# Kernel tuning notes

Measured on AMD Instinct MI355X. Metric: run time of the kernel, lower is better.

The kernel has to match this reference:

```python
import jax, jax.numpy as jnp
import numpy as np

N_IMG = 8
IMG_H = IMG_W = 1024
STRIDES = (4, 8, 16, 32, 64)
FEAT = tuple(IMG_H // s for s in STRIDES)
RATIOS = (0.5, 1.0, 2.0)
A = len(RATIOS)
PRE_NMS = 1000
POST_NMS = 1000
NMS_THRESH = 0.7
SCORE_THRESH = 0.0
MIN_SIZE = 1e-3
BBOX_CLIP = float(np.log(1000.0 / 16.0))  # torchvision bbox_xform_clip
NPL = tuple(f * f * A for f in FEAT)      # anchors per level


def _make_anchors():
    levels = []
    for stride, f in zip(STRIDES, FEAT):
        size = stride * 8.0
        base = []
        for r in RATIOS:
            w = size * np.sqrt(1.0 / r)
            h = size * np.sqrt(r)
            base.append([-w / 2, -h / 2, w / 2, h / 2])
        base = np.asarray(base, np.float32)              # [A,4]
        coords = np.arange(f, dtype=np.float32) * stride
        sy, sx = np.meshgrid(coords, coords, indexing="ij")
        shifts = np.stack([sx, sy, sx, sy], -1).reshape(-1, 1, 4)  # y-major, matches [H,W,A] flatten
        levels.append((shifts + base[None]).reshape(-1, 4))
    return np.concatenate(levels, 0).astype(np.float32)


def setup_inputs() -> dict:
    key = jax.random.key(0)
    ks = jax.random.split(key, 10)
    inp = {}
    for i, f in enumerate(FEAT):
        inp[f"obj_l{i}"] = jax.random.normal(ks[i], (N_IMG, A, f, f), jnp.float32)
        inp[f"delta_l{i}"] = jax.random.normal(ks[5 + i], (N_IMG, A * 4, f, f), jnp.float32) * 0.2
    inp["anchors"] = jnp.asarray(_make_anchors())
    return inp


def _flatten_level(obj, delta):
    # permute_and_flatten: [N,A,H,W] -> [N,H*W*A] ; [N,A*4,H,W] -> [N,H*W*A,4]
    n, a, h, w = obj.shape
    o = jnp.transpose(obj, (0, 2, 3, 1)).reshape(n, -1)
    d = jnp.transpose(delta.reshape(n, a, 4, h, w), (0, 3, 4, 1, 2)).reshape(n, -1, 4)
    return o, d


def _decode(deltas, anchors):
    # BoxCoder(weights=(1,1,1,1)).decode
    w = anchors[:, 2] - anchors[:, 0]
    h = anchors[:, 3] - anchors[:, 1]
    cx = anchors[:, 0] + 0.5 * w
    cy = anchors[:, 1] + 0.5 * h
    dx, dy = deltas[..., 0], deltas[..., 1]
    dw = jnp.minimum(deltas[..., 2], BBOX_CLIP)
    dh = jnp.minimum(deltas[..., 3], BBOX_CLIP)
    pcx = dx * w + cx
    pcy = dy * h + cy
    pw = jnp.exp(dw) * w
    ph = jnp.exp(dh) * h
    return jnp.stack([pcx - 0.5 * pw, pcy - 0.5 * ph, pcx + 0.5 * pw, pcy + 0.5 * ph], -1)


def _nms_image(boxes, scores, lvl):
    # clip_boxes_to_image
    x1 = jnp.clip(boxes[:, 0], 0.0, IMG_W)
    y1 = jnp.clip(boxes[:, 1], 0.0, IMG_H)
    x2 = jnp.clip(boxes[:, 2], 0.0, IMG_W)
    y2 = jnp.clip(boxes[:, 3], 0.0, IMG_H)
    boxes = jnp.stack([x1, y1, x2, y2], -1)
    # remove_small_boxes + score_thresh, as a mask (fixed shapes)
    valid = (x2 - x1 >= MIN_SIZE) & (y2 - y1 >= MIN_SIZE) & (scores >= SCORE_THRESH)
    s = jnp.where(valid, scores, -1.0)
    order = jnp.argsort(-s)
    boxes, s, valid, lvl = boxes[order], s[order], valid[order], lvl[order]
    # batched_nms: offset boxes per level so cross-level IoU is 0
    ob = boxes + (lvl.astype(boxes.dtype) * (max(IMG_H, IMG_W) + 1.0))[:, None]
    ob = jax.lax.stop_gradient(ob)  # keep decisions are non-differentiable
    area = (ob[:, 2] - ob[:, 0]) * (ob[:, 3] - ob[:, 1])
    lt = jnp.maximum(ob[:, None, :2], ob[None, :, :2])
    rb = jnp.minimum(ob[:, None, 2:], ob[None, :, 2:])
    wh = jnp.maximum(rb - lt, 0.0)
    inter = wh[..., 0] * wh[..., 1]
    iou = inter / (area[:, None] + area[None, :] - inter + 1e-9)  # [K,K]
    k = boxes.shape[0]
    jidx = jnp.arange(k)

    def body(i, keep):
        sup = keep[i] & (iou[i] > NMS_THRESH) & (jidx > i)
        return keep & ~sup

    keep = jax.lax.fori_loop(0, k, body, valid)
    # compact kept boxes (score-sorted) into fixed [POST_NMS] output, zero-padded
    rank = jnp.cumsum(keep) - 1
    tgt = jnp.where(keep & (rank < POST_NMS), rank, POST_NMS)
    out_b = jnp.zeros((POST_NMS + 1, 4), boxes.dtype).at[tgt].set(boxes)[:POST_NMS]
    out_s = jnp.zeros((POST_NMS + 1,), s.dtype).at[tgt].set(jnp.where(keep, s, 0.0))[:POST_NMS]
    return out_b, out_s


def _forward(objs, deltas, anchors):
    flat = [_flatten_level(o, d) for o, d in zip(objs, deltas)]
    obj = jnp.concatenate([f[0] for f in flat], 1)       # [N, K_total]
    dl = jnp.concatenate([f[1] for f in flat], 1)        # [N, K_total, 4]
    proposals = _decode(dl, anchors)                     # [N, K_total, 4]
    lvl_full = jnp.concatenate([jnp.full((n,), i, jnp.int32) for i, n in enumerate(NPL)])
    # per-level top-k on objectness logits
    idxs, off = [], 0
    for n in NPL:
        kk = min(PRE_NMS, n)
        _, ti = jax.lax.top_k(obj[:, off:off + n], kk)
        idxs.append(ti + off)
        off += n
    top_idx = jnp.concatenate(idxs, 1)                   # [N, K_sel]
    scores = jax.nn.sigmoid(jnp.take_along_axis(obj, top_idx, 1))
    prop = jnp.take_along_axis(proposals, top_idx[..., None], 1)
    lvl = lvl_full[top_idx]
    boxes_out, _ = jax.lax.map(lambda t: _nms_image(*t), (prop, scores, lvl))
    return boxes_out                                     # [N, POST_NMS, 4]


def reference(obj_l0, obj_l1, obj_l2, obj_l3, obj_l4, delta_l0, delta_l1, delta_l2, delta_l3, delta_l4, anchors):
    return _forward([obj_l0, obj_l1, obj_l2, obj_l3, obj_l4],
                    [delta_l0, delta_l1, delta_l2, delta_l3, delta_l4], anchors)
```

## Files before the change

### kernel.cpp

```cpp
#include <hip/hip_runtime.h>
#include <cstdint>

#define K_SEL 4768
#define CAND_CAP 16384
#define NBIN 4096
#define BUFCAP 512

struct P5 { const float* p[5]; };

__device__ __forceinline__ unsigned fsortkey(float f) {
  unsigned b = __float_as_uint(f);
  return (b & 0x80000000u) ? ~b : (b | 0x80000000u);
}

__global__ __launch_bounds__(256) void k_hist(P5 obj, unsigned* phist) {
  int p = blockIdx.y; int img = p / 5, lvl = p % 5;
  int f = 256 >> lvl; int n = 3 * f * f;
  __shared__ unsigned lh[NBIN];
  for (int b = threadIdx.x; b < NBIN; b += 256) lh[b] = 0;
  __syncthreads();
  const float4* src4 = (const float4*)(obj.p[lvl] + (size_t)img * n);
  int n4 = n >> 2;
  int chunk = (n4 + gridDim.x - 1) / gridDim.x;
  int e0 = blockIdx.x * chunk, e1 = min(n4, e0 + chunk);
  for (int e = e0 + threadIdx.x; e < e1; e += 256) {
    float4 v = src4[e];
    atomicAdd(&lh[fsortkey(v.x) >> 20], 1u);
    atomicAdd(&lh[fsortkey(v.y) >> 20], 1u);
    atomicAdd(&lh[fsortkey(v.z) >> 20], 1u);
    atomicAdd(&lh[fsortkey(v.w) >> 20], 1u);
  }
  __syncthreads();
  unsigned* dst = phist + ((size_t)(p * 8 + blockIdx.x)) * NBIN;
  for (int b = threadIdx.x; b < NBIN; b += 256) dst[b] = lh[b];
}

__global__ __launch_bounds__(256) void k_thresh(const unsigned* phist, int* Bthr, unsigned* cnt) {
  int p = blockIdx.x; int lvl = p % 5;
  unsigned kk = (lvl == 4) ? 768u : 1000u;
  __shared__ unsigned hsum[NBIN];
  __shared__ unsigned csum[256];
  int c = threadIdx.x;
  unsigned tot[16];
#pragma unroll
  for (int k = 0; k < 16; ++k) tot[k] = 0;
  for (int g = 0; g < 8; ++g) {
    const unsigned* hp = phist + ((size_t)(p * 8 + g)) * NBIN + c * 16;
#pragma unroll
    for (int k = 0; k < 16; ++k) tot[k] += hp[k];
  }
  unsigned s = 0;
#pragma unroll
  for (int k = 0; k < 16; ++k) { hsum[c * 16 + k] = tot[k]; s += tot[k]; }
  csum[c] = s;
  __syncthreads();
  if (c == 0) {
    unsigned acc = 0; int B = 0;
    for (int cc = 255; cc >= 0; --cc) {
      if (acc + csum[cc] >= kk) {
        for (int b = 15; b >= 0; --b) {
          acc += hsum[cc * 16 + b];
          if (acc >= kk) { B = cc * 16 + b; break; }
        }
        break;
      }
      acc += csum[cc];
    }
    Bthr[p] = B;
    cnt[p] = 0;
  }
}

__global__ __launch_bounds__(256) void k_gather(P5 obj, const int* Bthr, unsigned* cnt,
                                                unsigned long long* ck) {
  int p = blockIdx.y; int img = p / 5, lvl = p % 5;
  int f = 256 >> lvl; int hw = f * f; int n = 3 * hw;
  int B = Bthr[p];
  int shift = 2 * (8 - lvl);
  const float4* src4 = (const float4*)(obj.p[lvl] + (size_t)img * n);
  int n4 = n >> 2;
  unsigned long long* dst = ck + (size_t)p * CAND_CAP;
  int tid = threadIdx.x;
  int lane = tid & 63, wv = tid >> 6;
  __shared__ unsigned long long buf[4][BUFCAP];
  __shared__ unsigned wTot[4];
  __shared__ unsigned blkBase;
  unsigned wc = 0;
  for (int e = blockIdx.x * 256 + tid; e < n4; e += gridDim.x * 256) {
    float4 v = src4[e];
    float vv[4] = {v.x, v.y, v.z, v.w};
#pragma unroll
    for (int j = 0; j < 4; ++j) {
      unsigned sv = fsortkey(vv[j]);
      bool pass = (int)(sv >> 20) >= B;
      unsigned long long m = __ballot(pass);
      if (m) {
        if (pass) {
          unsigned pos = wc + (unsigned)__popcll(m & ((1ULL << lane) - 1ULL));
          int ee = e * 4 + j;
          int a = ee >> shift;
          int r = ee & (hw - 1);
          unsigned kidx = (unsigned)(r * 3 + a);
          unsigned long long key = ((unsigned long long)sv << 32) | (0xFFFFFFFFu - kidx);
          if (pos < BUFCAP) buf[wv][pos] = key;
          else {
            unsigned gp = atomicAdd(&cnt[p], 1u);
            if (gp < CAND_CAP) dst[gp] = key;
          }
        }
        wc += (unsigned)__popcll(m);
      }
    }
  }
  if (lane == 0) wTot[wv] = min(wc, (unsigned)BUFCAP);
  __syncthreads();
  if (tid == 0) {
    unsigned tot = wTot[0] + wTot[1] + wTot[2] + wTot[3];
    blkBase = tot ? atomicAdd(&cnt[p], tot) : 0u;
  }
  __syncthreads();
  unsigned myOff = blkBase;
  for (int x = 0; x < wv; ++x) myOff += wTot[x];
  unsigned wn = wTot[wv];
  for (unsigned j = lane; j < wn; j += 64) {
    unsigned gp = myOff + j;
    if (gp < CAND_CAP) dst[gp] = buf[wv][j];
  }
}

__global__ __launch_bounds__(256) void k_select(const unsigned* cnt, const unsigned long long* ck,
                                                unsigned* selSV, unsigned* selIdx) {
  int p = blockIdx.y; int img = p / 5, lvl = p % 5;
  int Cc = min((int)cnt[p], CAND_CAP);
  if (blockIdx.x * 256 >= Cc) return;
  int kk = (lvl == 4) ? 768 : 1000;
  int soff = lvl * 1000;
  const unsigned long long* keys = ck + (size_t)p * CAND_CAP;
  __shared__ unsigned long long sk[4096];
  int stage = min(Cc, 4096);
  for (int j = threadIdx.x; j < stage; j += 256) sk[j] = keys[j];
  __syncthreads();
  int c = blockIdx.x * 256 + threadIdx.x;
  if (c >= Cc) return;
  unsigned long long kc = keys[c];
  int rank = 0;
#pragma unroll 8
  for (int j = 0; j < stage; ++j) rank += (sk[j] > kc) ? 1 : 0;
  for (int j = stage; j < Cc; ++j) rank += (keys[j] > kc) ? 1 : 0;
  if (rank < kk) {
    int slot = img * K_SEL + soff + rank;
    selSV[slot]  = (unsigned)(kc >> 32);
    selIdx[slot] = 0xFFFFFFFFu - (unsigned)kc;
  }
}

__global__ __launch_bounds__(256) void k_decode(P5 del, const float* anchors,
                                                const unsigned* selSV, const unsigned* selIdx,
                                                float* boxP, unsigned long long* keyP) {
  int i = blockIdx.x * 256 + threadIdx.x;
  if (i >= K_SEL) return;
  int img = blockIdx.y;
  int lvl = (i < 4000) ? (i / 1000) : 4;
  int f = 256 >> lvl, hw = f * f;
  const int aoffA[5] = {0, 196608, 245760, 258048, 261120};
  int slot = img * K_SEL + i;
  unsigned k = selIdx[slot];
  unsigned sv = selSV[slot];
  int a = (int)(k % 3u); int r = (int)(k / 3u);
  int y = r >> (8 - lvl); int x = r & (f - 1);
  const float* dp = del.p[lvl] + (size_t)(img * 12 + a * 4) * hw + (size_t)y * f + x;
  float d0 = dp[0], d1 = dp[hw], d2 = dp[2 * hw], d3 = dp[3 * hw];
  const float* ar = anchors + (size_t)(aoffA[lvl] + (int)k) * 4;
  float a0 = ar[0], a1 = ar[1], a2 = ar[2], a3 = ar[3];
  float w = __fsub_rn(a2, a0), h = __fsub_rn(a3, a1);
  float cx = __fadd_rn(a0, __fmul_rn(0.5f, w));
  float cy = __fadd_rn(a1, __fmul_rn(0.5f, h));
  const float CLIP = 4.135166556742356f;
  float dw = fminf(d2, CLIP), dh = fminf(d3, CLIP);
  float pcx = __fadd_rn(__fmul_rn(d0, w), cx);
  float pcy = __fadd_rn(__fmul_rn(d1, h), cy);
  float pw = __fmul_rn(expf(dw), w);
  float ph = __fmul_rn(expf(dh), h);
  float x1 = __fsub_rn(pcx, __fmul_rn(0.5f, pw));
  float y1 = __fsub_rn(pcy, __fmul_rn(0.5f, ph));
  float x2 = __fadd_rn(pcx, __fmul_rn(0.5f, pw));
  float y2 = __fadd_rn(pcy, __fmul_rn(0.5f, ph));
  float x1c = fminf(fmaxf(x1, 0.0f), 1024.0f);
  float y1c = fminf(fmaxf(y1, 0.0f), 1024.0f);
  float x2c = fminf(fmaxf(x2, 0.0f), 1024.0f);
  float y2c = fminf(fmaxf(y2, 0.0f), 1024.0f);
  bool valid = (__fsub_rn(x2c, x1c) >= 1e-3f) && (__fsub_rn(y2c, y1c) >= 1e-3f);
  float* bp = boxP + (size_t)slot * 4;
  bp[0] = x1c; bp[1] = y1c; bp[2] = x2c; bp[3] = y2c;
  unsigned low = 0xFFFFFFFFu - (unsigned)i;
  keyP[slot] = valid ? (((unsigned long long)sv << 32) | low) : (unsigned long long)low;
}

__device__ __forceinline__ bool iou_gt(float rx1, float ry1, float rx2, float ry2, float rar,
                                       float cx1, float cy1, float cx2, float cy2, float car) {
  float ltx = fmaxf(rx1, cx1), lty = fmaxf(ry1, cy1);
  float rbx = fminf(rx2, cx2), rby = fminf(ry2, cy2);
  float wx = fmaxf(__fsub_rn(rbx, ltx), 0.0f);
  float wy = fmaxf(__fsub_rn(rby, lty), 0.0f);
  float inter = __fmul_rn(wx, wy);
  float denom = __fadd_rn(__fsub_rn(__fadd_rn(rar, car), inter), 1e-9f);
  return __fdiv_rn(inter, denom) > 0.7f;
}

__global__ __launch_bounds__(64) void k_lvlmask(const float* boxP, unsigned long long* gmask,
                                                unsigned long long* diagT) {
  int img = blockIdx.y;
  int q = blockIdx.x;
  int lvl, q2;
  if (q < 544) { lvl = q / 136; q2 = q - lvl * 136; }
  else         { lvl = 4;       q2 = q - 544; }
  int kk = (lvl == 4) ? 768 : 1000;
  int nch = (kk + 63) >> 6;
  int rb = 0;
  while (q2 >= nch - rb) { q2 -= nch - rb; ++rb; }
  int cb = rb + q2;
  int t = threadIdx.x;
  float off = __fmul_rn((float)lvl, 1025.0f);
  const float4* b4 = (const float4*)boxP + (size_t)img * K_SEL + lvl * 1000;
  __shared__ float cx1[64], cy1[64], cx2[64], cy2[64], car[64];
  int j = cb * 64 + t;
  if (j < kk) {
    float4 bb = b4[j];
    float ox1 = __fadd_rn(bb.x, off), oy1 = __fadd_rn(bb.y, off);
    float ox2 = __fadd_rn(bb.z, off), oy2 = __fadd_rn(bb.w, off);
    cx1[t] = ox1; cy1[t] = oy1; cx2[t] = ox2; cy2[t] = oy2;
    car[t] = __fmul_rn(__fsub_rn(ox2, ox1), __fsub_rn(oy2, oy1));
  }
  __syncthreads();
  int i = rb * 64 + t;
  if (i >= kk) return;
  float4 bb = b4[i];
  float rx1 = __fadd_rn(bb.x, off), ry1 = __fadd_rn(bb.y, off);
  float rx2 = __fadd_rn(bb.z, off), ry2 = __fadd_rn(bb.w, off);
  float rar = __fmul_rn(__fsub_rn(rx2, rx1), __fsub_rn(ry2, ry1));
  unsigned long long bits = 0;
  int jmax = min(64, kk - cb * 64);
  if (rb == cb) {
    unsigned long long bitsT = 0;
    for (int jj = 0; jj < jmax; ++jj) {
      if (jj == t) continue;
      if (iou_gt(rx1, ry1, rx2, ry2, rar, cx1[jj], cy1[jj], cx2[jj], cy2[jj], car[jj])) {
        if (jj > t) bits  |= (1ULL << jj);
        else        bitsT |= (1ULL << jj);
      }
    }
    diagT[((size_t)(img * 5 + lvl) * 16 + rb) * 64 + t] = bitsT;
  } else {
    for (int jj = 0; jj < jmax; ++jj) {
      if (iou_gt(rx1, ry1, rx2, ry2, rar, cx1[jj], cy1[jj], cx2[jj], cy2[jj], car[jj]))
        bits |= (1ULL << jj);
    }
  }
  gmask[((size_t)(img * 5 + lvl) * 1000 + i) * 16 + cb] = bits;
}

__global__ __launch_bounds__(64, 1) void k_lvlnms(const unsigned long long* keyP,
                                                  const unsigned long long* gmask,
                                                  const unsigned long long* diagT,
                                                  unsigned long long* keepw) {
  int p = blockIdx.x; int img = p / 5, lvl = p % 5;
  int kk = (lvl == 4) ? 768 : 1000;
  int nch = (kk + 63) >> 6;
  int t = threadIdx.x;
  int g = t >> 4, w = t & 15;
  const unsigned long long* gm = gmask + (size_t)p * 16000;
  const unsigned long long* kp = keyP + (size_t)img * K_SEL + lvl * 1000;
  const unsigned long long* dT = diagT + (size_t)p * (16 * 64);
  unsigned long long rp = 0ULL;
  int i0 = min(t, kk - 1);
  unsigned long long vpre = kp[i0];
  unsigned long long tpre = dT[t];
  for (int c = 0; c < nch; ++c) {
    int cbase = c * 64;
    const unsigned long long* sb = gm + (size_t)(cbase + g) * 16 + w;
    unsigned long long spec[16];
#pragma unroll
    for (int k = 0; k < 16; ++k) spec[k] = sb[k * 64];
    int i = cbase + t;
    bool inb = i < kk;
    bool cand0 = inb && (vpre >> 32) != 0ULL;
    unsigned long long colT = tpre;
    int cn = (c + 1 < nch) ? c + 1 : c;
    int inx = min(cn * 64 + t, kk - 1);
    vpre = kp[inx];
    tpre = dT[cn * 64 + t];
    unsigned long long cur = __shfl(rp, c) | __shfl(rp, 16 + c) |
                             __shfl(rp, 32 + c) | __shfl(rp, 48 + c);
    bool alive = cand0 && !((cur >> t) & 1ULL);
    unsigned long long keepm = 0ULL;
    unsigned long long actm = __ballot(alive);
    while (actm) {
      bool cank = alive && ((colT & actm) == 0ULL);
      unsigned long long newk = __ballot(cank);
      keepm |= newk;
      alive = alive && !cank && ((colT & newk) == 0ULL);
      actm = __ballot(alive);
    }
    if (t == 0) keepw[(size_t)p * 16 + c] = keepm;
    if (c + 1 == nch) break;
#pragma unroll
    for (int k = 0; k < 16; ++k)
      rp |= ((keepm >> (4 * k + g)) & 1ULL) ? spec[k] : 0ULL;
  }
}

__global__ __launch_bounds__(256) void k_merge(const unsigned long long* keyP, const float* boxP,
                                               const unsigned long long* keepw, float* out) {
  int p = blockIdx.x; int img = p / 5, lvl = p % 5;
  int tid = threadIdx.x;
  __shared__ unsigned long long lkey[5000];
  __shared__ int lpos[5000];
  __shared__ int wp[5][17];
  __shared__ unsigned long long kwS[80];
  for (int x = tid; x < 80; x += 256) {
    int l = x >> 4, w = x & 15;
    kwS[x] = (l == 4 && w >= 12) ? 0ULL : keepw[(size_t)img * 80 + x];
  }
  __syncthreads();
  if (tid < 5) {
    int acc = 0;
    for (int w = 0; w < 16; ++w) { wp[tid][w] = acc; acc += (int)__popcll(kwS[tid * 16 + w]); }
    wp[tid][16] = acc;
  }
  __syncthreads();
  const unsigned long long* kp = keyP + (size_t)img * K_SEL;
  for (int i = tid; i < K_SEL; i += 256) {
    int l = (i < 4000) ? i / 1000 : 4;
    int li = i - l * 1000;
    unsigned long long wmask = kwS[l * 16 + (li >> 6)];
    if ((wmask >> (li & 63)) & 1ULL) {
      int j = wp[l][li >> 6] + (int)__popcll(wmask & ((1ULL << (li & 63)) - 1ULL));
      lkey[l * 1000 + j] = kp[i];
      lpos[l * 1000 + j] = i;
    }
  }
  __syncthreads();
  const float4* b4 = (const float4*)boxP + (size_t)img * K_SEL;
  float4* out4 = (float4*)out + (size_t)img * 1000;
  int kn = wp[lvl][16];
  for (int j = tid; j < kn; j += 256) {
    unsigned long long key = lkey[lvl * 1000 + j];
    int grank = j;
#pragma unroll
    for (int l2 = 0; l2 < 5; ++l2) {
      if (l2 == lvl) continue;
      int lo = 0, hi = wp[l2][16];
      const unsigned long long* a = &lkey[l2 * 1000];
      while (lo < hi) { int mid = (lo + hi) >> 1; if (a[mid] > key) lo = mid + 1; else hi = mid; }
      grank += lo;
    }
    if (grank < 1000) out4[grank] = b4[lpos[lvl * 1000 + j]];
  }
  if (lvl == 0) {
    int KT = wp[0][16] + wp[1][16] + wp[2][16] + wp[3][16] + wp[4][16];
    for (int s = min(KT, 1000) + tid; s < 1000; s += 256)
      out4[s] = make_float4(0.f, 0.f, 0.f, 0.f);
  }
}

extern "C" void kernel_launch(void* const* d_in, const int* in_sizes, int n_in,
                              void* d_out, int out_size, void* d_ws, size_t ws_size,
                              hipStream_t stream) {
  (void)in_sizes; (void)n_in;
  P5 obj, del;
  for (int i = 0; i < 5; ++i) {
    obj.p[i] = (const float*)d_in[2 * i];
    del.p[i] = (const float*)d_in[2 * i + 1];
  }
  const float* anchors = (const float*)d_in[10];
  float* out = (float*)d_out;
  char* ws = (char*)d_ws;

  unsigned* cnt               = (unsigned*)(ws + 0);
  int* Bthr                   = (int*)(ws + 192);
  unsigned long long* candK   = (unsigned long long*)(ws + 512);
  unsigned* selSV             = (unsigned*)(ws + 5243392);
  unsigned* selIdx            = (unsigned*)(ws + 5395968);
  float* boxP                 = (float*)(ws + 5548544);
  unsigned long long* keyP    = (unsigned long long*)(ws + 6158848);
  unsigned long long* keepw   = (unsigned long long*)(ws + 6464000);
  unsigned long long* gmask   = (unsigned long long*)(ws + 6469120);
  unsigned* phist             = (unsigned*)(ws + 6469120);
  unsigned long long* diagT   = (unsigned long long*)(ws + 512);
  const size_t NEED = 11712000ULL;
  if (ws_size < NEED) { hipMemsetAsync(d_out, 0, (size_t)out_size * 4, stream); return; }

  k_hist    <<<dim3(8, 40), 256, 0, stream>>>(obj, phist);
  k_thresh  <<<40, 256, 0, stream>>>(phist, Bthr, cnt);
  k_gather  <<<dim3(32, 40), 256, 0, stream>>>(obj, Bthr, cnt, candK);
  k_select  <<<dim3(64, 40), 256, 0, stream>>>(cnt, candK, selSV, selIdx);
  k_decode  <<<dim3(19, 8), 256, 0, stream>>>(del, anchors, selSV, selIdx, boxP, keyP);
  k_lvlmask <<<dim3(622, 8), 64, 0, stream>>>(boxP, gmask, diagT);
  k_lvlnms  <<<40, 64, 0, stream>>>(keyP, gmask, diagT, keepw);
  k_merge   <<<40, 256, 0, stream>>>(keyP, boxP, keepw, out);
}
```

Before: 226.0 us.

## Replace sequential chunked NMS with parallel fixed-point NMS over lower-triangular suppression bitmask

The mask kernel now writes only the lower-triangular suppressor bits (earlier boxes that overlap each box) into a packed, padded triangular layout, and drops the separate diagonal-transpose buffer. The per-level NMS kernel becomes a 256-thread block that loads the triangular mask into LDS. It then iterates a parallel fixed point: a box is kept when no undecided or kept predecessor suppresses it, and dead when a kept one does. This replaces the serial 64-box chunk walk, trading serial latency for repeated rounds whose count depends on suppression-chain depth, plus a large LDS footprint per block.

```diff
diff --git a/kernel.cpp b/kernel.cpp
--- a/kernel.cpp
+++ b/kernel.cpp
@@ -5,6 +5,7 @@
 #define CAND_CAP 16384
 #define NBIN 4096
 #define BUFCAP 512
+#define TPAD 9216
 
 struct P5 { const float* p[5]; };
 
@@ -207,8 +208,7 @@
   return __fdiv_rn(inter, denom) > 0.7f;
 }
 
-__global__ __launch_bounds__(64) void k_lvlmask(const float* boxP, unsigned long long* gmask,
-                                                unsigned long long* diagT) {
+__global__ __launch_bounds__(64) void k_lvlmask(const float* boxP, unsigned long long* T) {
   int img = blockIdx.y;
   int q = blockIdx.x;
   int lvl, q2;
@@ -222,91 +222,91 @@
   int t = threadIdx.x;
   float off = __fmul_rn((float)lvl, 1025.0f);
   const float4* b4 = (const float4*)boxP + (size_t)img * K_SEL + lvl * 1000;
-  __shared__ float cx1[64], cy1[64], cx2[64], cy2[64], car[64];
-  int j = cb * 64 + t;
+  __shared__ float rx1s[64], ry1s[64], rx2s[64], ry2s[64], rars[64];
+  int j = rb * 64 + t;
   if (j < kk) {
     float4 bb = b4[j];
     float ox1 = __fadd_rn(bb.x, off), oy1 = __fadd_rn(bb.y, off);
     float ox2 = __fadd_rn(bb.z, off), oy2 = __fadd_rn(bb.w, off);
-    cx1[t] = ox1; cy1[t] = oy1; cx2[t] = ox2; cy2[t] = oy2;
-    car[t] = __fmul_rn(__fsub_rn(ox2, ox1), __fsub_rn(oy2, oy1));
-  }
-  __syncthreads();
-  int i = rb * 64 + t;
+    rx1s[t] = ox1; ry1s[t] = oy1; rx2s[t] = ox2; ry2s[t] = oy2;
+    rars[t] = __fmul_rn(__fsub_rn(ox2, ox1), __fsub_rn(oy2, oy1));
+  }
+  __syncthreads();
+  int i = cb * 64 + t;
   if (i >= kk) return;
   float4 bb = b4[i];
-  float rx1 = __fadd_rn(bb.x, off), ry1 = __fadd_rn(bb.y, off);
-  float rx2 = __fadd_rn(bb.z, off), ry2 = __fadd_rn(bb.w, off);
-  float rar = __fmul_rn(__fsub_rn(rx2, rx1), __fsub_rn(ry2, ry1));
+  float cx1 = __fadd_rn(bb.x, off), cy1 = __fadd_rn(bb.y, off);
+  float cx2 = __fadd_rn(bb.z, off), cy2 = __fadd_rn(bb.w, off);
+  float car = __fmul_rn(__fsub_rn(cx2, cx1), __fsub_rn(cy2, cy1));
+  int jmaxR = min(64, kk - rb * 64);
+  int jend = (rb == cb) ? min(t, jmaxR) : jmaxR;
   unsigned long long bits = 0;
-  int jmax = min(64, kk - cb * 64);
-  if (rb == cb) {
-    unsigned long long bitsT = 0;
-    for (int jj = 0; jj < jmax; ++jj) {
-      if (jj == t) continue;
-      if (iou_gt(rx1, ry1, rx2, ry2, rar, cx1[jj], cy1[jj], cx2[jj], cy2[jj], car[jj])) {
-        if (jj > t) bits  |= (1ULL << jj);
-        else        bitsT |= (1ULL << jj);
-      }
-    }
-    diagT[((size_t)(img * 5 + lvl) * 16 + rb) * 64 + t] = bitsT;
-  } else {
-    for (int jj = 0; jj < jmax; ++jj) {
-      if (iou_gt(rx1, ry1, rx2, ry2, rar, cx1[jj], cy1[jj], cx2[jj], cy2[jj], car[jj]))
-        bits |= (1ULL << jj);
-    }
-  }
-  gmask[((size_t)(img * 5 + lvl) * 1000 + i) * 16 + cb] = bits;
-}
-
-__global__ __launch_bounds__(64, 1) void k_lvlnms(const unsigned long long* keyP,
-                                                  const unsigned long long* gmask,
-                                                  const unsigned long long* diagT,
-                                                  unsigned long long* keepw) {
+  for (int jj = 0; jj < jend; ++jj) {
+    if (iou_gt(rx1s[jj], ry1s[jj], rx2s[jj], ry2s[jj], rars[jj], cx1, cy1, cx2, cy2, car))
+      bits |= (1ULL << jj);
+  }
+  const int Pt[16] = {0, 1, 4, 7, 12, 17, 24, 31, 40, 49, 60, 71, 84, 97, 112, 127};
+  int sc = (cb + 1) | 1;
+  T[(size_t)(img * 5 + lvl) * TPAD + 64 * Pt[cb] + t * sc + rb] = bits;
+}
+
+__global__ __launch_bounds__(256) void k_lvlnms(const unsigned long long* keyP,
+                                                const unsigned long long* Tg_,
+                                                unsigned long long* keepw) {
   int p = blockIdx.x; int img = p / 5, lvl = p % 5;
   int kk = (lvl == 4) ? 768 : 1000;
-  int nch = (kk + 63) >> 6;
-  int t = threadIdx.x;
-  int g = t >> 4, w = t & 15;
-  const unsigned long long* gm = gmask + (size_t)p * 16000;
+  int tw = (lvl == 4) ? 5376 : TPAD;
+  int tid = threadIdx.x;
+  int lane = tid & 63, wv = tid >> 6;
+  __shared__ __align__(16) unsigned long long Ts[TPAD];
+  __shared__ unsigned long long Us[16], Ks[16];
+  const unsigned long long* Tg = Tg_ + (size_t)p * TPAD;
+  for (int x = tid; x < (tw >> 1); x += 256)
+    ((ulonglong2*)Ts)[x] = ((const ulonglong2*)Tg)[x];
   const unsigned long long* kp = keyP + (size_t)img * K_SEL + lvl * 1000;
-  const unsigned long long* dT = diagT + (size_t)p * (16 * 64);
-  unsigned long long rp = 0ULL;
-  int i0 = min(t, kk - 1);
-  unsigned long long vpre = kp[i0];
-  unsigned long long tpre = dT[t];
-  for (int c = 0; c < nch; ++c) {
-    int cbase = c * 64;
-    const unsigned long long* sb = gm + (size_t)(cbase + g) * 16 + w;
-    unsigned long long spec[16];
-#pragma unroll
-    for (int k = 0; k < 16; ++k) spec[k] = sb[k * 64];
-    int i = cbase + t;
-    bool inb = i < kk;
-    bool cand0 = inb && (vpre >> 32) != 0ULL;
-    unsigned long long colT = tpre;
-    int cn = (c + 1 < nch) ? c + 1 : c;
-    int inx = min(cn * 64 + t, kk - 1);
-    vpre = kp[inx];
-    tpre = dT[cn * 64 + t];
-    unsigned long long cur = __shfl(rp, c) | __shfl(rp, 16 + c) |
-                             __shfl(rp, 32 + c) | __shfl(rp, 48 + c);
-    bool alive = cand0 && !((cur >> t) & 1ULL);
-    unsigned long long keepm = 0ULL;
-    unsigned long long actm = __ballot(alive);
-    while (actm) {
-      bool cank = alive && ((colT & actm) == 0ULL);
-      unsigned long long newk = __ballot(cank);
-      keepm |= newk;
-      alive = alive && !cank && ((colT & newk) == 0ULL);
-      actm = __ballot(alive);
-    }
-    if (t == 0) keepw[(size_t)p * 16 + c] = keepm;
-    if (c + 1 == nch) break;
-#pragma unroll
-    for (int k = 0; k < 16; ++k)
-      rp |= ((keepm >> (4 * k + g)) & 1ULL) ? spec[k] : 0ULL;
-  }
+#pragma unroll
+  for (int jb = 0; jb < 4; ++jb) {
+    int i = jb * 256 + tid;
+    bool valid = (i < kk) && ((kp[min(i, kk - 1)] >> 32) != 0ULL);
+    unsigned long long m = __ballot(valid);
+    if (lane == 0) { int wi = jb * 4 + wv; Us[wi] = m; Ks[wi] = 0ULL; }
+  }
+  __syncthreads();
+  const int Pt[16] = {0, 1, 4, 7, 12, 17, 24, 31, 40, 49, 60, 71, 84, 97, 112, 127};
+  while (true) {
+    unsigned long long us[16], ks[16], ku[16], uAny = 0;
+#pragma unroll
+    for (int w = 0; w < 16; ++w) {
+      us[w] = Us[w]; ks[w] = Ks[w]; ku[w] = us[w] | ks[w]; uAny |= us[w];
+    }
+    __syncthreads();
+    if (uAny == 0ULL) break;
+#pragma unroll
+    for (int jb = 0; jb < 4; ++jb) {
+      int i = jb * 256 + tid;
+      bool inU = (i < kk) && ((us[i >> 6] >> (i & 63)) & 1ULL);
+      bool kept = false, dead = false;
+      if (inU) {
+        int ci = i >> 6, il = i & 63;
+        int base = 64 * Pt[ci] + il * ((ci + 1) | 1);
+        unsigned long long a = 0, b = 0;
+        for (int w = 0; w <= ci; ++w) {
+          unsigned long long tv = Ts[base + w];
+          a |= tv & ku[w]; b |= tv & ks[w];
+        }
+        kept = (a == 0ULL);
+        dead = !kept && (b != 0ULL);
+      }
+      unsigned long long mk = __ballot(kept), md = __ballot(dead);
+      if (lane == 0) {
+        int wi = jb * 4 + wv;
+        Ks[wi] |= mk;
+        Us[wi] &= ~(mk | md);
+      }
+    }
+    __syncthreads();
+  }
+  if (tid < 16) keepw[(size_t)p * 16 + tid] = Ks[tid];
 }
 
 __global__ __launch_bounds__(256) void k_merge(const unsigned long long* keyP, const float* boxP,
@@ -384,9 +384,8 @@
   float* boxP                 = (float*)(ws + 5548544);
   unsigned long long* keyP    = (unsigned long long*)(ws + 6158848);
   unsigned long long* keepw   = (unsigned long long*)(ws + 6464000);
-  unsigned long long* gmask   = (unsigned long long*)(ws + 6469120);
+  unsigned long long* T       = (unsigned long long*)(ws + 6469120);
   unsigned* phist             = (unsigned*)(ws + 6469120);
-  unsigned long long* diagT   = (unsigned long long*)(ws + 512);
   const size_t NEED = 11712000ULL;
   if (ws_size < NEED) { hipMemsetAsync(d_out, 0, (size_t)out_size * 4, stream); return; }
 
@@ -395,7 +394,7 @@
   k_gather  <<<dim3(32, 40), 256, 0, stream>>>(obj, Bthr, cnt, candK);
   k_select  <<<dim3(64, 40), 256, 0, stream>>>(cnt, candK, selSV, selIdx);
   k_decode  <<<dim3(19, 8), 256, 0, stream>>>(del, anchors, selSV, selIdx, boxP, keyP);
-  k_lvlmask <<<dim3(622, 8), 64, 0, stream>>>(boxP, gmask, diagT);
-  k_lvlnms  <<<40, 64, 0, stream>>>(keyP, gmask, diagT, keepw);
+  k_lvlmask <<<dim3(622, 8), 64, 0, stream>>>(boxP, T);
+  k_lvlnms  <<<40, 256, 0, stream>>>(keyP, T, keepw);
   k_merge   <<<40, 256, 0, stream>>>(keyP, boxP, keepw, out);
 }
```

Measured after the change: 251.1 us. 11.1% more time.
